# Kernel optimization log

Measured on AMD Instinct MI355X. Metric: run time of the kernel, lower is better.

Reference implementation:

```python
import jax, jax.numpy as jnp
import numpy as np
from jax import lax

H = 32  # hidden_dim

def _lstm_layer(x_tbd, W_ih, W_hh, b_ih, b_hh):
    """x_tbd: [T, B, D]. Returns all hidden states [T, B, H]. PyTorch gate order i,f,g,o."""
    T, B, _ = x_tbd.shape
    # Precompute input contribution for all timesteps (one big GEMM)
    xW = jnp.einsum('tbd,gd->tbg', x_tbd, W_ih) + (b_ih + b_hh)  # [T, B, 4H]
    W_hh_T = W_hh.T  # [H, 4H]

    def step(carry, xw):
        h, c = carry
        gates = xw + h @ W_hh_T  # [B, 4H]
        i, f, g, o = jnp.split(gates, 4, axis=-1)
        i = jax.nn.sigmoid(i)
        f = jax.nn.sigmoid(f)
        g = jnp.tanh(g)
        o = jax.nn.sigmoid(o)
        c = f * c + i * g
        h = o * jnp.tanh(c)
        return (h, c), h

    h0 = jnp.zeros((B, H), x_tbd.dtype)
    (_, _), hs = lax.scan(step, (h0, h0), xW)
    return hs  # [T, B, H]


def setup_inputs() -> dict:
    key = jax.random.key(0)
    ks = jax.random.split(key, 12)
    s = 0.1  # keep gates out of saturation
    return {
        'x': jax.random.normal(ks[0], (4096, 512, 4), jnp.float32),
        'W_ih0': jax.random.normal(ks[1], (4 * H, 4), jnp.float32) * s,
        'W_hh0': jax.random.normal(ks[2], (4 * H, H), jnp.float32) * s,
        'b_ih0': jax.random.normal(ks[3], (4 * H,), jnp.float32) * s,
        'b_hh0': jax.random.normal(ks[4], (4 * H,), jnp.float32) * s,
        'W_ih1': jax.random.normal(ks[5], (4 * H, H), jnp.float32) * s,
        'W_hh1': jax.random.normal(ks[6], (4 * H, H), jnp.float32) * s,
        'b_ih1': jax.random.normal(ks[7], (4 * H,), jnp.float32) * s,
        'b_hh1': jax.random.normal(ks[8], (4 * H,), jnp.float32) * s,
        'W_out': jax.random.normal(ks[9], (1, H), jnp.float32) * s,
        'b_out': jax.random.normal(ks[10], (1,), jnp.float32) * s,
    }


def reference(x, W_ih0, W_hh0, b_ih0, b_hh0, W_ih1, W_hh1, b_ih1, b_hh1, W_out, b_out):
    # x: [B, T, D] (batch_first). Eval mode -> inter-layer dropout is identity.
    x_tbd = jnp.transpose(x, (1, 0, 2))  # [T, B, D]
    h1 = _lstm_layer(x_tbd, W_ih0, W_hh0, b_ih0, b_hh0)  # [T, B, H]
    h2 = _lstm_layer(h1, W_ih1, W_hh1, b_ih1, b_hh1)     # [T, B, H]
    last = h2[-1]  # [B, H] == out[:, -1, :]
    return last @ W_out.T + b_out  # [B, 1]
```

## Files before the change

### kernel.cpp

```cpp
#include <hip/hip_runtime.h>
#include <cmath>

constexpr int T   = 512;
constexpr int D   = 4;
constexpr int H   = 32;
constexpr int BT  = 16;
constexpr int BLK = 512;

constexpr float LOG2E     = 1.44269504088896340736f;
constexpr float NEG2LOG2E = -2.88539008177792681472f;

constexpr int XSTRIDE = 4104;
constexpr int HSTR = 40;

typedef short bf8 __attribute__((ext_vector_type(8)));
typedef float f4  __attribute__((ext_vector_type(4)));
typedef float f2  __attribute__((ext_vector_type(2)));

static __device__ __forceinline__ short bf16_rtn(float v) {
    unsigned u = __float_as_uint(v);
    u += 0x7FFFu + ((u >> 16) & 1u);
    return (short)(u >> 16);
}

__global__ __launch_bounds__(BLK, 1) void lstm_bf16p(
    const float* __restrict__ x,
    const float* __restrict__ W_ih0, const float* __restrict__ W_hh0,
    const float* __restrict__ b_ih0, const float* __restrict__ b_hh0,
    const float* __restrict__ W_ih1, const float* __restrict__ W_hh1,
    const float* __restrict__ b_ih1, const float* __restrict__ b_hh1,
    const float* __restrict__ W_out, const float* __restrict__ b_out,
    float* __restrict__ out)
{
    __shared__ __align__(16) short xbf[16 * XSTRIDE];
    __shared__ __align__(16) short h0b[2][16][HSTR];
    __shared__ __align__(16) short h1b[2][16][HSTR];
    __shared__ __align__(16) float h1f[16][36];

    const int tid   = threadIdx.x;
    const int w     = tid >> 6;
    const int lane  = tid & 63;
    const int q     = lane >> 4;
    const int nl    = lane & 15;
    const int rsel  = w >> 2;
    const int wl    = w & 3;
    const int layer = wl >> 1;
    const int ug    = (wl & 1) << 4;
    const int b0    = blockIdx.x * BT;

    for (int idx = tid; idx < 16 * T; idx += BLK) {
        const int col = idx & 15;
        const int t   = idx >> 4;
        float4 xv = *(const float4*)(x + ((size_t)(b0 + col) * T + t) * D);
        bf8 v = {0, 0, 0, 0, 0, 0, 0, 0};
        v[0] = bf16_rtn(xv.x); v[1] = bf16_rtn(xv.y);
        v[2] = bf16_rtn(xv.z); v[3] = bf16_rtn(xv.w);
        *(bf8*)&xbf[col * XSTRIDE + t * 8] = v;
    }
    for (int idx = tid; idx < 2 * 16 * HSTR; idx += BLK) {
        (&h0b[0][0][0])[idx] = 0;
        (&h1b[0][0][0])[idx] = 0;
    }

    const float* W1 = layer ? W_ih1 : W_hh0;
    bf8 w1[4], w2[4];
    f4  bias[4];
    #pragma unroll
    for (int g = 0; g < 4; ++g) {
        const float sc = (g == 2) ? NEG2LOG2E : -LOG2E;
        const int row = 32 * g + ug + nl;
        #pragma unroll
        for (int j = 0; j < 8; ++j) {
            w1[g][j] = bf16_rtn(W1[row * H + 8 * q + j] * sc);
            float v2 = layer ? W_hh1[row * H + 8 * q + j]
                             : ((q == 0 && j < 4) ? W_ih0[row * D + j] : 0.0f);
            w2[g][j] = bf16_rtn(v2 * sc);
        }
        #pragma unroll
        for (int r = 0; r < 4; ++r) {
            const int gr = 32 * g + ug + 4 * q + r;
            bias[g][r] = sc * (layer ? (b_ih1[gr] + b_hh1[gr])
                                     : (b_ih0[gr] + b_hh0[gr]));
        }
    }

    f2 c2; c2.x = 0.0f; c2.y = 0.0f;

    const short* xcol = &xbf[nl * XSTRIDE];

    __syncthreads();

    auto actpair = [&](float zi0, float zi1, float zf0, float zf1,
                       float zg0, float zg1, float zo0, float zo1,
                       unsigned& pkd, f2& hv) {
        f2 ei, ef, eg, eo, ec;
        ei.x = __builtin_amdgcn_exp2f(zi0); ei.y = __builtin_amdgcn_exp2f(zi1);
        ef.x = __builtin_amdgcn_exp2f(zf0); ef.y = __builtin_amdgcn_exp2f(zf1);
        eg.x = __builtin_amdgcn_exp2f(zg0); eg.y = __builtin_amdgcn_exp2f(zg1);
        eo.x = __builtin_amdgcn_exp2f(zo0); eo.y = __builtin_amdgcn_exp2f(zo1);
        f2 D1 = 1.0f + ef;
        f2 D2 = (1.0f + ei) * (1.0f + eg);
        f2 Dm = D1 * D2;
        float R = __builtin_amdgcn_rcpf(Dm.x * Dm.y);
        f2 rD; rD.x = R * Dm.y; rD.y = R * Dm.x;
        c2 = (c2 * D2 + (1.0f - eg) * D1) * rD;
        ec.x = __builtin_amdgcn_exp2f(c2.x * NEG2LOG2E);
        ec.y = __builtin_amdgcn_exp2f(c2.y * NEG2LOG2E);
        f2 Do = (1.0f + eo) * (1.0f + ec);
        float Ro = __builtin_amdgcn_rcpf(Do.x * Do.y);
        f2 ro; ro.x = Ro * Do.y; ro.y = Ro * Do.x;
        hv = (1.0f - ec) * ro;
        asm("v_cvt_pk_bf16_f32 %0, %1, %2" : "=v"(pkd) : "v"(hv.x), "v"(hv.y));
    };

    auto body = [&](const int i, const int rb, const int wb) {
        bf8 b2;
        if (layer == 0) {
            b2 = *(const bf8*)&xcol[(i & (T - 1)) * 8];
        } else {
            b2 = *(const bf8*)&h1b[rb][nl][8 * q];
        }
        bf8 b1 = *(const bf8*)&h0b[rb][nl][8 * q];

        f4 acc[4];
        #pragma unroll
        for (int g = 0; g < 4; ++g) {
            f4 A = __builtin_amdgcn_mfma_f32_16x16x32_bf16(w2[g], b2, bias[g], 0, 0, 0);
            A    = __builtin_amdgcn_mfma_f32_16x16x32_bf16(w1[g], b1, A,       0, 0, 0);
            acc[g] = A;
        }

        const bool act = layer ? (i >= 1) : (i < T);
        if (act) {
            unsigned pk; f2 hv;
            if (rsel == 0) {
                actpair(acc[0][0], acc[0][1], acc[1][0], acc[1][1],
                        acc[2][0], acc[2][1], acc[3][0], acc[3][1], pk, hv);
            } else {
                actpair(acc[0][2], acc[0][3], acc[1][2], acc[1][3],
                        acc[2][2], acc[2][3], acc[3][2], acc[3][3], pk, hv);
            }
            short* hb = layer ? &h1b[wb][nl][0] : &h0b[wb][nl][0];
            *(unsigned*)&hb[ug + 4 * q + 2 * rsel] = pk;
            if (layer && i == T) {
                float2 hw; hw.x = hv.x; hw.y = hv.y;
                *(float2*)&h1f[nl][ug + 4 * q + 2 * rsel] = hw;
            }
        }
        __syncthreads();
    };

    #pragma unroll 1
    for (int i = 0; i < T; i += 2) {
        body(i,     0, 1);
        body(i + 1, 1, 0);
    }
    body(T, 0, 1);

    if (tid < BT) {
        float acc = b_out[0];
        #pragma unroll
        for (int u = 0; u < H; ++u) acc = fmaf(W_out[u], h1f[tid][u], acc);
        out[b0 + tid] = acc;
    }
}

extern "C" void kernel_launch(void* const* d_in, const int* in_sizes, int n_in,
                              void* d_out, int out_size, void* d_ws, size_t ws_size,
                              hipStream_t stream) {
    const float* x     = (const float*)d_in[0];
    const float* W_ih0 = (const float*)d_in[1];
    const float* W_hh0 = (const float*)d_in[2];
    const float* b_ih0 = (const float*)d_in[3];
    const float* b_hh0 = (const float*)d_in[4];
    const float* W_ih1 = (const float*)d_in[5];
    const float* W_hh1 = (const float*)d_in[6];
    const float* b_ih1 = (const float*)d_in[7];
    const float* b_hh1 = (const float*)d_in[8];
    const float* W_out = (const float*)d_in[9];
    const float* b_out = (const float*)d_in[10];
    float* out = (float*)d_out;

    const int B = out_size;
    lstm_bf16p<<<B / BT, BLK, 0, stream>>>(x, W_ih0, W_hh0, b_ih0, b_hh0,
                                           W_ih1, W_hh1, b_ih1, b_hh1,
                                           W_out, b_out, out);
}
```

Before: 282.5 us.

## Run each LSTM layer in one wave with lagged layer-1 and batched barriers

The block shrinks from 8 waves to 2: one wave computes all 32 hidden units of layer 0, the other computes layer 1. Layer 1 runs 8 timesteps behind layer 0. Layer-0 hidden states go into a 16-slot ring buffer, so the two waves only need a block barrier every 8 steps instead of every step. Intra-wave ordering is relied on for each wave's own recurrence. In exchange each wave now does 4x the MFMA and activation work per step serially, and fewer waves are available to hide latency.

```diff
diff --git a/kernel.cpp b/kernel.cpp
--- a/kernel.cpp
+++ b/kernel.cpp
@@ -5,7 +5,9 @@
 constexpr int D   = 4;
 constexpr int H   = 32;
 constexpr int BT  = 16;
-constexpr int BLK = 512;
+constexpr int BLK = 128;
+constexpr int LAG = 8;
+constexpr int NS  = 16;
 
 constexpr float LOG2E     = 1.44269504088896340736f;
 constexpr float NEG2LOG2E = -2.88539008177792681472f;
@@ -23,7 +25,7 @@
     return (short)(u >> 16);
 }
 
-__global__ __launch_bounds__(BLK, 1) void lstm_bf16p(
+__global__ __launch_bounds__(BLK, 1) void lstm_wl(
     const float* __restrict__ x,
     const float* __restrict__ W_ih0, const float* __restrict__ W_hh0,
     const float* __restrict__ b_ih0, const float* __restrict__ b_hh0,
@@ -33,20 +35,16 @@
     float* __restrict__ out)
 {
     __shared__ __align__(16) short xbf[16 * XSTRIDE];
-    __shared__ __align__(16) short h0b[2][16][HSTR];
-    __shared__ __align__(16) short h1b[2][16][HSTR];
+    __shared__ __align__(16) short h0r[NS][16][HSTR];
+    __shared__ __align__(16) short h1d[2][16][HSTR];
     __shared__ __align__(16) float h1f[16][36];
 
-    const int tid   = threadIdx.x;
-    const int w     = tid >> 6;
-    const int lane  = tid & 63;
-    const int q     = lane >> 4;
-    const int nl    = lane & 15;
-    const int rsel  = w >> 2;
-    const int wl    = w & 3;
-    const int layer = wl >> 1;
-    const int ug    = (wl & 1) << 4;
-    const int b0    = blockIdx.x * BT;
+    const int tid  = threadIdx.x;
+    const int isL0 = (tid < 64);
+    const int lane = tid & 63;
+    const int q    = lane >> 4;
+    const int nl   = lane & 15;
+    const int b0   = blockIdx.x * BT;
 
     for (int idx = tid; idx < 16 * T; idx += BLK) {
         const int col = idx & 15;
@@ -57,40 +55,42 @@
         v[2] = bf16_rtn(xv.z); v[3] = bf16_rtn(xv.w);
         *(bf8*)&xbf[col * XSTRIDE + t * 8] = v;
     }
-    for (int idx = tid; idx < 2 * 16 * HSTR; idx += BLK) {
-        (&h0b[0][0][0])[idx] = 0;
-        (&h1b[0][0][0])[idx] = 0;
-    }
-
-    const float* W1 = layer ? W_ih1 : W_hh0;
-    bf8 w1[4], w2[4];
-    f4  bias[4];
+    for (int idx = tid; idx < NS * 16 * HSTR; idx += BLK) (&h0r[0][0][0])[idx] = 0;
+    for (int idx = tid; idx < 2 * 16 * HSTR; idx += BLK) (&h1d[0][0][0])[idx] = 0;
+
+    const float* W1 = isL0 ? W_hh0 : W_ih1;
+    bf8 w1[4][2], w2[4][2];
+    f4  bias[4][2];
     #pragma unroll
     for (int g = 0; g < 4; ++g) {
         const float sc = (g == 2) ? NEG2LOG2E : -LOG2E;
-        const int row = 32 * g + ug + nl;
         #pragma unroll
-        for (int j = 0; j < 8; ++j) {
-            w1[g][j] = bf16_rtn(W1[row * H + 8 * q + j] * sc);
-            float v2 = layer ? W_hh1[row * H + 8 * q + j]
-                             : ((q == 0 && j < 4) ? W_ih0[row * D + j] : 0.0f);
-            w2[g][j] = bf16_rtn(v2 * sc);
-        }
-        #pragma unroll
-        for (int r = 0; r < 4; ++r) {
-            const int gr = 32 * g + ug + 4 * q + r;
-            bias[g][r] = sc * (layer ? (b_ih1[gr] + b_hh1[gr])
-                                     : (b_ih0[gr] + b_hh0[gr]));
+        for (int hf = 0; hf < 2; ++hf) {
+            const int row = 32 * g + 16 * hf + nl;
+            #pragma unroll
+            for (int j = 0; j < 8; ++j) {
+                w1[g][hf][j] = bf16_rtn(W1[row * H + 8 * q + j] * sc);
+                float v2 = isL0 ? ((q == 0 && j < 4) ? W_ih0[row * D + j] : 0.0f)
+                                : W_hh1[row * H + 8 * q + j];
+                w2[g][hf][j] = bf16_rtn(v2 * sc);
+            }
+            #pragma unroll
+            for (int r = 0; r < 4; ++r) {
+                const int gr = 32 * g + 16 * hf + 4 * q + r;
+                bias[g][hf][r] = sc * (isL0 ? (b_ih0[gr] + b_hh0[gr])
+                                            : (b_ih1[gr] + b_hh1[gr]));
+            }
         }
     }
 
-    f2 c2; c2.x = 0.0f; c2.y = 0.0f;
+    f2 cs[2][2];
+    cs[0][0] = 0.0f; cs[0][1] = 0.0f; cs[1][0] = 0.0f; cs[1][1] = 0.0f;
 
     const short* xcol = &xbf[nl * XSTRIDE];
 
     __syncthreads();
 
-    auto actpair = [&](float zi0, float zi1, float zf0, float zf1,
+    auto actpair = [&](f2& c2, float zi0, float zi1, float zf0, float zf1,
                        float zg0, float zg1, float zo0, float zo1,
                        unsigned& pkd, f2& hv) {
         f2 ei, ef, eg, eo, ec;
@@ -113,49 +113,84 @@
         asm("v_cvt_pk_bf16_f32 %0, %1, %2" : "=v"(pkd) : "v"(hv.x), "v"(hv.y));
     };
 
-    auto body = [&](const int i, const int rb, const int wb) {
-        bf8 b2;
-        if (layer == 0) {
-            b2 = *(const bf8*)&xcol[(i & (T - 1)) * 8];
-        } else {
-            b2 = *(const bf8*)&h1b[rb][nl][8 * q];
-        }
-        bf8 b1 = *(const bf8*)&h0b[rb][nl][8 * q];
-
-        f4 acc[4];
+    auto group8 = [&](const int t0, const int sbase, const bool do0, const bool do1) {
         #pragma unroll
-        for (int g = 0; g < 4; ++g) {
-            f4 A = __builtin_amdgcn_mfma_f32_16x16x32_bf16(w2[g], b2, bias[g], 0, 0, 0);
-            A    = __builtin_amdgcn_mfma_f32_16x16x32_bf16(w1[g], b1, A,       0, 0, 0);
-            acc[g] = A;
-        }
-
-        const bool act = layer ? (i >= 1) : (i < T);
-        if (act) {
-            unsigned pk; f2 hv;
-            if (rsel == 0) {
-                actpair(acc[0][0], acc[0][1], acc[1][0], acc[1][1],
-                        acc[2][0], acc[2][1], acc[3][0], acc[3][1], pk, hv);
-            } else {
-                actpair(acc[0][2], acc[0][3], acc[1][2], acc[1][3],
-                        acc[2][2], acc[2][3], acc[3][2], acc[3][3], pk, hv);
-            }
-            short* hb = layer ? &h1b[wb][nl][0] : &h0b[wb][nl][0];
-            *(unsigned*)&hb[ug + 4 * q + 2 * rsel] = pk;
-            if (layer && i == T) {
-                float2 hw; hw.x = hv.x; hw.y = hv.y;
-                *(float2*)&h1f[nl][ug + 4 * q + 2 * rsel] = hw;
+        for (int u = 0; u < 8; ++u) {
+            if (do0 && isL0) {
+                bf8 b2 = *(const bf8*)&xcol[(t0 + u) * 8];
+                const int sr = (sbase + u - 1) & (NS - 1);
+                bf8 b1 = *(const bf8*)&h0r[sr][nl][8 * q];
+                f4 acc[4][2];
+                #pragma unroll
+                for (int g = 0; g < 4; ++g)
+                    #pragma unroll
+                    for (int hf = 0; hf < 2; ++hf) {
+                        f4 A = __builtin_amdgcn_mfma_f32_16x16x32_bf16(w2[g][hf], b2, bias[g][hf], 0, 0, 0);
+                        acc[g][hf] = __builtin_amdgcn_mfma_f32_16x16x32_bf16(w1[g][hf], b1, A, 0, 0, 0);
+                    }
+                unsigned pka, pkb; f2 hv;
+                const int sw = sbase + u;
+                actpair(cs[0][0], acc[0][0][0], acc[0][0][1], acc[1][0][0], acc[1][0][1],
+                        acc[2][0][0], acc[2][0][1], acc[3][0][0], acc[3][0][1], pka, hv);
+                actpair(cs[0][1], acc[0][0][2], acc[0][0][3], acc[1][0][2], acc[1][0][3],
+                        acc[2][0][2], acc[2][0][3], acc[3][0][2], acc[3][0][3], pkb, hv);
+                int2 wlo; wlo.x = (int)pka; wlo.y = (int)pkb;
+                *(int2*)&h0r[sw][nl][4 * q] = wlo;
+                actpair(cs[1][0], acc[0][1][0], acc[0][1][1], acc[1][1][0], acc[1][1][1],
+                        acc[2][1][0], acc[2][1][1], acc[3][1][0], acc[3][1][1], pka, hv);
+                actpair(cs[1][1], acc[0][1][2], acc[0][1][3], acc[1][1][2], acc[1][1][3],
+                        acc[2][1][2], acc[2][1][3], acc[3][1][2], acc[3][1][3], pkb, hv);
+                int2 whi; whi.x = (int)pka; whi.y = (int)pkb;
+                *(int2*)&h0r[sw][nl][16 + 4 * q] = whi;
+            }
+            if (do1 && !isL0) {
+                const int jj = t0 + u - LAG;
+                const int wb = u & 1;
+                const int rb = wb ^ 1;
+                const int sb = (sbase + u + 8) & (NS - 1);
+                bf8 b1 = *(const bf8*)&h0r[sb][nl][8 * q];
+                bf8 b2 = *(const bf8*)&h1d[rb][nl][8 * q];
+                f4 acc[4][2];
+                #pragma unroll
+                for (int g = 0; g < 4; ++g)
+                    #pragma unroll
+                    for (int hf = 0; hf < 2; ++hf) {
+                        f4 A = __builtin_amdgcn_mfma_f32_16x16x32_bf16(w2[g][hf], b2, bias[g][hf], 0, 0, 0);
+                        acc[g][hf] = __builtin_amdgcn_mfma_f32_16x16x32_bf16(w1[g][hf], b1, A, 0, 0, 0);
+                    }
+                unsigned pka, pkb; f2 hv0, hv1, hv2, hv3;
+                actpair(cs[0][0], acc[0][0][0], acc[0][0][1], acc[1][0][0], acc[1][0][1],
+                        acc[2][0][0], acc[2][0][1], acc[3][0][0], acc[3][0][1], pka, hv0);
+                actpair(cs[0][1], acc[0][0][2], acc[0][0][3], acc[1][0][2], acc[1][0][3],
+                        acc[2][0][2], acc[2][0][3], acc[3][0][2], acc[3][0][3], pkb, hv1);
+                int2 wlo; wlo.x = (int)pka; wlo.y = (int)pkb;
+                *(int2*)&h1d[wb][nl][4 * q] = wlo;
+                actpair(cs[1][0], acc[0][1][0], acc[0][1][1], acc[1][1][0], acc[1][1][1],
+                        acc[2][1][0], acc[2][1][1], acc[3][1][0], acc[3][1][1], pka, hv2);
+                actpair(cs[1][1], acc[0][1][2], acc[0][1][3], acc[1][1][2], acc[1][1][3],
+                        acc[2][1][2], acc[2][1][3], acc[3][1][2], acc[3][1][3], pkb, hv3);
+                int2 whi; whi.x = (int)pka; whi.y = (int)pkb;
+                *(int2*)&h1d[wb][nl][16 + 4 * q] = whi;
+                if (jj == T - 1) {
+                    float2 a; a.x = hv0.x; a.y = hv0.y;
+                    float2 b; b.x = hv1.x; b.y = hv1.y;
+                    float2 c; c.x = hv2.x; c.y = hv2.y;
+                    float2 d; d.x = hv3.x; d.y = hv3.y;
+                    *(float2*)&h1f[nl][4 * q]          = a;
+                    *(float2*)&h1f[nl][4 * q + 2]      = b;
+                    *(float2*)&h1f[nl][16 + 4 * q]     = c;
+                    *(float2*)&h1f[nl][16 + 4 * q + 2] = d;
+                }
             }
         }
         __syncthreads();
     };
 
+    group8(0, 0, true, false);
     #pragma unroll 1
-    for (int i = 0; i < T; i += 2) {
-        body(i,     0, 1);
-        body(i + 1, 1, 0);
-    }
-    body(T, 0, 1);
+    for (int g = 1; g < 64; ++g)
+        group8(8 * g, (g & 1) * 8, true, true);
+    group8(T, 0, false, true);
 
     if (tid < BT) {
         float acc = b_out[0];
@@ -182,7 +217,7 @@
     float* out = (float*)d_out;
 
     const int B = out_size;
-    lstm_bf16p<<<B / BT, BLK, 0, stream>>>(x, W_ih0, W_hh0, b_ih0, b_hh0,
-                                           W_ih1, W_hh1, b_ih1, b_hh1,
-                                           W_out, b_out, out);
+    lstm_wl<<<B / BT, BLK, 0, stream>>>(x, W_ih0, W_hh0, b_ih0, b_hh0,
+                                        W_ih1, W_hh1, b_ih1, b_hh1,
+                                        W_out, b_out, out);
 }
```

New measurement: 429.3 us. 52.0% more time.
